# Optimization experiments

Hardware: AMD Instinct MI355X
Metric: run time of the kernel (lower is better)

The kernel has to match this reference:

```python
import jax, jax.numpy as jnp
import numpy as np

N, P, C, S, H, CLS = 32, 16, 256, 128, 4, 3000
DH = C // H
EPS = 1e-5


def setup_inputs() -> dict:
    key = jax.random.key(0)
    ks = jax.random.split(key, 8)
    sh = (N, P, C, S)
    return {
        "t_f": jax.random.normal(ks[0], sh, jnp.float32),
        "t_s": jax.random.normal(ks[1], sh, jnp.float32),
        "t_l": jax.random.normal(ks[2], sh, jnp.float32),
        # grouped 1x1 conv weights, one [out_ch, in_ch] matrix per part
        "decay_w": jax.random.normal(ks[3], (P, C, 3 * C), jnp.float32) * 0.02,
        "qkv_w": jax.random.normal(ks[4], (P, 3 * C, C), jnp.float32) * 0.02,
        "out_w": jax.random.normal(ks[5], (P, C, C), jnp.float32) * 0.02,
        # per-part BatchNorm1d affine params
        "gamma": jnp.ones((P, C), jnp.float32),
        "beta": jnp.zeros((P, C), jnp.float32),
        # classifier fc: [in_planes, class_num] (broadcast over parts)
        "fc": jax.random.normal(ks[6], (C, CLS), jnp.float32) * 0.02,
    }


def reference(t_f, t_s, t_l, decay_w, qkv_w, out_w, gamma, beta, fc):
    n, p, c, s = t_f.shape
    h, dh = H, DH
    scale = dh ** -0.5

    # decay_c: grouped 1x1 conv, 3c -> c per part
    x_cat = jnp.concatenate([t_f, t_s, t_l], axis=2)            # [n,p,3c,s]
    t_all = jnp.einsum('npis,poi->npos', x_cat, decay_w)        # [n,p,c,s]

    # Attention.to_qkv: grouped 1x1 conv, c -> 3c per part
    qkv = jnp.einsum('npcs,pqc->npqs', t_all, qkv_w)            # [n,p,3c,s]
    qkv = qkv.reshape(n, p, 3, h, dh, s).transpose(2, 0, 3, 1, 4, 5)  # [3,n,h,p,dh,s]
    q, k, v = qkv[0], qkv[1], qkv[2]

    # frame-frame attention per (head, part): [n,h,p,s,s]
    dots = jnp.einsum('nhpcs,nhpct->nhpst', q, k) * scale
    attn = jax.nn.softmax(dots, axis=-1)

    o = jnp.einsum('nhpst,nhpct->nhpcs', attn, v)               # [n,h,p,dh,s]
    o = o.transpose(0, 2, 1, 3, 4).reshape(n, p, c, s)          # [n,p,c,s]
    o = jnp.einsum('npcs,poc->npos', o, out_w)                  # to_out grouped conv

    # residual + max over frames
    wpv = (o + t_all).max(axis=-1)                              # [n,p,c]

    # select_topk_part (topk_num == 1 forced by squeeze(2) in torch code):
    # argmax over frames of column-summed attention, gather that frame of t_f, sum heads
    idx = jnp.argmax(attn.sum(axis=-2), axis=-1)                # [n,h,p]
    ib = jnp.broadcast_to(idx[:, :, :, None, None], (n, h, p, c, 1))
    sel = jnp.take_along_axis(t_f[:, None], ib, axis=-1)[..., 0]  # [n,h,p,c]
    sel = sel.sum(axis=1)                                       # [n,p,c]

    # per-part BatchNorm1d in training mode (batch statistics over n)
    mean = wpv.mean(axis=0)                                     # [p,c]
    var = wpv.var(axis=0)                                       # biased, as torch BN
    pf = (wpv - mean) / jnp.sqrt(var + EPS) * gamma + beta      # [n,p,c]

    cls = jnp.einsum('npc,ck->npk', pf, fc)                     # [n,p,class_num]
    return cls, wpv.transpose(1, 0, 2), sel.transpose(1, 0, 2)
```

## Files before the change

kernel.cpp:

```cpp
#include <hip/hip_runtime.h>
#include <math.h>

#define N_ 32
#define P_ 16
#define C_ 256
#define S_ 128
#define H_ 4
#define CLS_ 3000

typedef __attribute__((ext_vector_type(4))) float f4v;
typedef __attribute__((ext_vector_type(4))) float f32x4;
typedef __attribute__((ext_vector_type(8))) short short8;
typedef __attribute__((ext_vector_type(4))) unsigned short us4;

__device__ __forceinline__ unsigned short f2bf(float x){
    unsigned u = __float_as_uint(x);
    u += 0x7fffu + ((u >> 16) & 1u);
    return (unsigned short)(u >> 16);
}
__device__ __forceinline__ float bf2f(unsigned short h){
    return __uint_as_float(((unsigned)h) << 16);
}

typedef __attribute__((address_space(1))) const unsigned int gu32_t;
typedef __attribute__((address_space(3))) unsigned int lu32_t;
__device__ __forceinline__ void gload16(const void* g, void* l){
    __builtin_amdgcn_global_load_lds((gu32_t*)g, (lu32_t*)l, 16, 0, 0);
}

__global__ void wsplit(const float* __restrict__ dw, const float* __restrict__ qw,
                       const float* __restrict__ ow,
                       unsigned short* __restrict__ wdh, unsigned short* __restrict__ wdl,
                       unsigned short* __restrict__ wqh, unsigned short* __restrict__ wql,
                       unsigned short* __restrict__ woh){
    int i = blockIdx.x * 256 + threadIdx.x;
    int stride = gridDim.x * 256;
    for (; i < 3145728; i += stride){
        float a = dw[i]; unsigned short h = f2bf(a);
        wdh[i] = h; wdl[i] = f2bf(a - bf2f(h));
        float b = qw[i]; unsigned short h2 = f2bf(b);
        wqh[i] = h2; wql[i] = f2bf(b - bf2f(h2));
        if (i < 1048576) woh[i] = f2bf(ow[i]);
    }
}

__global__ __launch_bounds__(256) void fct_kernel(const float* __restrict__ fc,
                                                  unsigned short* __restrict__ fcT){
    int n = blockIdx.x * 256 + threadIdx.x;
    if (n < CLS_){
        for (int c = 0; c < 256; ++c) fcT[(size_t)n * 256 + c] = f2bf(fc[(size_t)c * CLS_ + n]);
    } else {
        for (int c = 0; c < 256; ++c) fcT[(size_t)n * 256 + c] = 0;
    }
}

__global__ __launch_bounds__(256) void xT_kernel(
    const float* __restrict__ t_f, const float* __restrict__ t_s,
    const float* __restrict__ t_l,
    unsigned short* __restrict__ xH, unsigned short* __restrict__ xL, int n0){
    __shared__ float T[64 * 132];
    const int np_l = blockIdx.x, tsel = blockIdx.y;
    const float* src = (tsel == 0) ? t_f : ((tsel == 1) ? t_s : t_l);
    const size_t np_g = (size_t)(n0 * 16) + np_l;
    const float* sbase = src + np_g * 256 * 128;
    const size_t dbase = (size_t)np_l * 128 * 768 + tsel * 256;
    const int tid = threadIdx.x;
    const int so = tid & 127, ch = tid >> 7;

    for (int cp = 0; cp < 4; ++cp){
        const int c0 = cp * 64;
#pragma unroll
        for (int it = 0; it < 8; ++it){
            int f = tid + 256 * it;
            int c = f >> 5, s4 = (f & 31) << 2;
            *(f4v*)(T + c * 132 + s4) = *(const f4v*)(sbase + (size_t)(c0 + c) * 128 + s4);
        }
        __syncthreads();
        short8 Hh[4], Ll[4];
#pragma unroll
        for (int c8 = 0; c8 < 4; ++c8){
#pragma unroll
            for (int j = 0; j < 8; ++j){
                float v = T[(ch * 32 + c8 * 8 + j) * 132 + so];
                unsigned short hh = f2bf(v);
                Hh[c8][j] = (short)hh;
                Ll[c8][j] = (short)f2bf(v - bf2f(hh));
            }
        }
        size_t dr = dbase + (size_t)so * 768 + c0 + ch * 32;
#pragma unroll
        for (int c8 = 0; c8 < 4; ++c8){
            *(short8*)(xH + dr + c8 * 8) = Hh[c8];
            *(short8*)(xL + dr + c8 * 8) = Ll[c8];
        }
        __syncthreads();
    }
}

template<int KEXT, int APITCH, int ND, int MODE, int OPITCH>
__global__ __launch_bounds__(256) void gemm3(
    const unsigned short* __restrict__ Ah_g, const unsigned short* __restrict__ Al_g,
    const unsigned short* __restrict__ Whi, const unsigned short* __restrict__ Wlo,
    const unsigned short* __restrict__ resH, const unsigned short* __restrict__ resL,
    unsigned short* __restrict__ outH, unsigned short* __restrict__ outL,
    float* __restrict__ outF, int n0, int cnp)
{
    constexpr int T3 = (MODE == 2) ? 0 : 1;
    constexpr int OB = ND / 128;
    __shared__ unsigned short sm[(T3 ? 4 : 2) * 128 * 64];
    unsigned short* AhL = sm;
    unsigned short* BhL = sm + 8192;
    unsigned short* AlL = T3 ? (sm + 16384) : sm;
    unsigned short* BlL = T3 ? (sm + 24576) : sm;
    unsigned short* Ep = sm;
    __shared__ float cmax[2][2][64];

    const int id = blockIdx.x;
    const int xcd = id & 7;
    const int r = id >> 3;
    const int ppl = r / (cnp * OB);
    const int rr = r % (cnp * OB);
    const int n_l = rr / OB;
    const int o_t = rr % OB;
    const int p = xcd * 2 + ppl;
    const int np_l = n_l * 16 + p;
    const int o0 = o_t * 128;

    const int tid = threadIdx.x;
    const int w = tid >> 6, l = tid & 63;
    const int lr = l & 15, lg = l >> 4;
    const int ws0 = (w & 1) * 64, wo0 = (w >> 1) * 64;
    const size_t aBase = (size_t)np_l * 128 * APITCH;
    const unsigned short* Wp_h = Whi + ((size_t)p * ND + o0) * KEXT;
    const unsigned short* Wp_l = T3 ? (Wlo + ((size_t)p * ND + o0) * KEXT) : Wp_h;

    f32x4 acc[4][4];
#pragma unroll
    for (int i = 0; i < 4; ++i)
#pragma unroll
        for (int j = 0; j < 4; ++j) acc[i][j] = (f32x4){0.f, 0.f, 0.f, 0.f};

    for (int k0 = 0; k0 < KEXT; k0 += 64){
#pragma unroll
        for (int it = 0; it < 4; ++it){
            int slot = w * 4 + it;
            int lin = slot * 64 + l;
            int row = lin >> 3, chnk = lin & 7;
            int sk = ((chnk ^ (row & 7)) << 3);
            unsigned short* ldst = sm + slot * 512;
            const unsigned short* ga = Ah_g + aBase + (size_t)row * APITCH + k0 + sk;
            gload16(ga, ldst);
            const unsigned short* gb = Wp_h + (size_t)row * KEXT + k0 + sk;
            gload16(gb, ldst + 8192);
            if (T3){
                gload16(Al_g + aBase + (size_t)row * APITCH + k0 + sk, ldst + 16384);
                gload16(Wp_l + (size_t)row * KEXT + k0 + sk, ldst + 24576);
            }
        }
        __syncthreads();
#pragma unroll
        for (int ks = 0; ks < 2; ++ks){
            short8 ah[4], al[4];
#pragma unroll
            for (int sf = 0; sf < 4; ++sf){
                int row = ws0 + sf * 16 + lr;
                int cof = ((ks * 4 + lg) ^ (row & 7)) << 3;
                ah[sf] = *(const short8*)(AhL + row * 64 + cof);
                if (T3) al[sf] = *(const short8*)(AlL + row * 64 + cof);
            }
#pragma unroll
            for (int of = 0; of < 4; ++of){
                int row = wo0 + of * 16 + lr;
                int cof = ((ks * 4 + lg) ^ (row & 7)) << 3;
                short8 bh = *(const short8*)(BhL + row * 64 + cof);
                short8 bl = bh;
                if (T3) bl = *(const short8*)(BlL + row * 64 + cof);
#pragma unroll
                for (int sf = 0; sf < 4; ++sf){
                    acc[sf][of] = __builtin_amdgcn_mfma_f32_16x16x32_bf16(ah[sf], bh, acc[sf][of], 0, 0, 0);
                    if (T3){
                        acc[sf][of] = __builtin_amdgcn_mfma_f32_16x16x32_bf16(ah[sf], bl, acc[sf][of], 0, 0, 0);
                        acc[sf][of] = __builtin_amdgcn_mfma_f32_16x16x32_bf16(al[sf], bh, acc[sf][of], 0, 0, 0);
                    }
                }
            }
        }
        __syncthreads();
    }

    if (MODE != 2){
#pragma unroll
        for (int plane = 0; plane < 2; ++plane){
#pragma unroll
            for (int sf = 0; sf < 4; ++sf)
#pragma unroll
                for (int of = 0; of < 4; ++of){
                    int col = wo0 + of * 16 + lr;
#pragma unroll
                    for (int r2 = 0; r2 < 4; ++r2){
                        int row = ws0 + sf * 16 + lg * 4 + r2;
                        float v = acc[sf][of][r2];
                        unsigned short hh = f2bf(v);
                        unsigned short q = plane ? f2bf(v - bf2f(hh)) : hh;
                        Ep[row * 136 + col] = q;
                    }
                }
            __syncthreads();
            unsigned short* dst = plane ? outL : outH;
#pragma unroll
            for (int it = 0; it < 8; ++it){
                int idx = tid + 256 * it;
                int row = idx >> 4, seg = (idx & 15) * 8;
                *(short8*)(dst + (size_t)np_l * 128 * OPITCH + (size_t)row * OPITCH + o0 + seg) =
                    *(const short8*)(Ep + row * 136 + seg);
            }
            __syncthreads();
        }
    } else {
        const int n_g = n0 + n_l;
#pragma unroll
        for (int of = 0; of < 4; ++of){
            int oc = o0 + wo0 + of * 16 + lr;
            float m = -INFINITY;
#pragma unroll
            for (int sf = 0; sf < 4; ++sf){
#pragma unroll
                for (int r2 = 0; r2 < 4; ++r2){
                    int s = ws0 + sf * 16 + lg * 4 + r2;
                    size_t ri = (size_t)np_l * 128 * 256 + (size_t)s * 256 + oc;
                    float v = acc[sf][of][r2] + bf2f(resH[ri]) + bf2f(resL[ri]);
                    m = fmaxf(m, v);
                }
            }
            m = fmaxf(m, __shfl_xor(m, 16));
            m = fmaxf(m, __shfl_xor(m, 32));
            if (l < 16) cmax[w >> 1][w & 1][of * 16 + l] = m;
        }
        __syncthreads();
        if (tid < 128){
            int oh = tid >> 6, col = tid & 63;
            float v = fmaxf(cmax[oh][0][col], cmax[oh][1][col]);
            outF[((size_t)p * N_ + n_g) * C_ + o0 + oh * 64 + col] = v;
        }
    }
}

__global__ __launch_bounds__(256) void attn3(unsigned short* __restrict__ qH,
                                             const unsigned short* __restrict__ qL,
                                             int* __restrict__ idxA, int n0, int cnp){
    __shared__ char smraw[17408 + 34816 + 2048];
    unsigned short* Vs = (unsigned short*)smraw;
    unsigned short* Pm = (unsigned short*)(smraw + 17408);
    float* csW = (float*)(smraw + 17408 + 34816);
    unsigned short* Ot = (unsigned short*)smraw;

    const int id = blockIdx.x;
    const int xcd = id & 7;
    const int r = id >> 3;
    const int ppl = r / (cnp * 4);
    const int rr = r % (cnp * 4);
    const int n_l = rr >> 2, h = rr & 3;
    const int p = xcd * 2 + ppl;
    const int np_l = n_l * 16 + p;
    const int tid = threadIdx.x, w = tid >> 6, l = tid & 63;
    const int lr = l & 15, lg = l >> 4;
    unsigned short* baseH = qH + (size_t)np_l * 128 * 768;
    const unsigned short* baseL = qL + (size_t)np_l * 128 * 768;

#pragma unroll
    for (int it = 0; it < 8; ++it){
        int idx = tid + 256 * it;
        int t = idx >> 4, d4 = (idx & 15) * 4;
        us4 v = *(const us4*)(baseH + (size_t)t * 768 + 512 + h * 64 + d4);
#pragma unroll
        for (int j = 0; j < 4; ++j) Vs[(d4 + j) * 136 + t] = v[j];
    }

    short8 qh[2][2], ql[2][2];
#pragma unroll
    for (int sf = 0; sf < 2; ++sf)
#pragma unroll
        for (int ks = 0; ks < 2; ++ks){
            size_t off = (size_t)(w * 32 + sf * 16 + lr) * 768 + h * 64 + ks * 32 + lg * 8;
            qh[sf][ks] = *(const short8*)(baseH + off);
            ql[sf][ks] = *(const short8*)(baseL + off);
        }

    f32x4 dacc[2][8];
#pragma unroll
    for (int i = 0; i < 2; ++i)
#pragma unroll
        for (int j = 0; j < 8; ++j) dacc[i][j] = (f32x4){0.f, 0.f, 0.f, 0.f};

#pragma unroll
    for (int tf = 0; tf < 8; ++tf){
#pragma unroll
        for (int ks = 0; ks < 2; ++ks){
            size_t off = (size_t)(tf * 16 + lr) * 768 + 256 + h * 64 + ks * 32 + lg * 8;
            short8 kh = *(const short8*)(baseH + off);
            short8 kl = *(const short8*)(baseL + off);
#pragma unroll
            for (int sf = 0; sf < 2; ++sf){
                dacc[sf][tf] = __builtin_amdgcn_mfma_f32_16x16x32_bf16(qh[sf][ks], kh, dacc[sf][tf], 0, 0, 0);
                dacc[sf][tf] = __builtin_amdgcn_mfma_f32_16x16x32_bf16(qh[sf][ks], kl, dacc[sf][tf], 0, 0, 0);
                dacc[sf][tf] = __builtin_amdgcn_mfma_f32_16x16x32_bf16(ql[sf][ks], kh, dacc[sf][tf], 0, 0, 0);
            }
        }
    }

    float csp[8];
#pragma unroll
    for (int tf = 0; tf < 8; ++tf) csp[tf] = 0.f;
#pragma unroll
    for (int sf = 0; sf < 2; ++sf){
#pragma unroll
        for (int r2 = 0; r2 < 4; ++r2){
            float m = -INFINITY;
#pragma unroll
            for (int tf = 0; tf < 8; ++tf) m = fmaxf(m, dacc[sf][tf][r2]);
            m = fmaxf(m, __shfl_xor(m, 1)); m = fmaxf(m, __shfl_xor(m, 2));
            m = fmaxf(m, __shfl_xor(m, 4)); m = fmaxf(m, __shfl_xor(m, 8));
            float e[8]; float sum = 0.f;
#pragma unroll
            for (int tf = 0; tf < 8; ++tf){
                e[tf] = __expf(0.125f * (dacc[sf][tf][r2] - m)); sum += e[tf];
            }
            sum += __shfl_xor(sum, 1); sum += __shfl_xor(sum, 2);
            sum += __shfl_xor(sum, 4); sum += __shfl_xor(sum, 8);
            float inv = 1.f / sum;
            int s = w * 32 + sf * 16 + lg * 4 + r2;
#pragma unroll
            for (int tf = 0; tf < 8; ++tf){
                float pv = e[tf] * inv;
                Pm[s * 136 + tf * 16 + lr] = f2bf(pv);
                csp[tf] += pv;
            }
        }
    }
#pragma unroll
    for (int tf = 0; tf < 8; ++tf){
        float v = csp[tf];
        v += __shfl_xor(v, 16); v += __shfl_xor(v, 32);
        if (l < 16) csW[w * 128 + tf * 16 + l] = v;
    }
    __syncthreads();

    f32x4 oacc[8];
#pragma unroll
    for (int i = 0; i < 8; ++i) oacc[i] = (f32x4){0.f, 0.f, 0.f, 0.f};
#pragma unroll
    for (int ks = 0; ks < 4; ++ks){
        short8 av = *(const short8*)(Vs + (w * 16 + lr) * 136 + ks * 32 + lg * 8);
#pragma unroll
        for (int sf = 0; sf < 8; ++sf){
            short8 bp = *(const short8*)(Pm + (sf * 16 + lr) * 136 + ks * 32 + lg * 8);
            oacc[sf] = __builtin_amdgcn_mfma_f32_16x16x32_bf16(av, bp, oacc[sf], 0, 0, 0);
        }
    }
    __syncthreads();

    if (tid < 64){
        float v0 = csW[tid] + csW[128 + tid] + csW[256 + tid] + csW[384 + tid];
        float v1 = csW[64 + tid] + csW[192 + tid] + csW[320 + tid] + csW[448 + tid];
        float bv; int bi;
        if (v1 > v0){ bv = v1; bi = 64 + tid; } else { bv = v0; bi = tid; }
#pragma unroll
        for (int msk = 1; msk <= 32; msk <<= 1){
            float ov = __shfl_xor(bv, msk); int oi = __shfl_xor(bi, msk);
            if (ov > bv || (ov == bv && oi < bi)){ bv = ov; bi = oi; }
        }
        if (tid == 0){ int n_g = n0 + n_l; idxA[(n_g * H_ + h) * P_ + p] = bi; }
    }

#pragma unroll
    for (int sf = 0; sf < 8; ++sf){
        int s = sf * 16 + lr;
#pragma unroll
        for (int r2 = 0; r2 < 4; ++r2) Ot[s * 72 + w * 16 + lg * 4 + r2] = f2bf(oacc[sf][r2]);
    }
    __syncthreads();
#pragma unroll
    for (int it = 0; it < 4; ++it){
        int idx = tid + 256 * it;
        int s = idx >> 3, d8 = (idx & 7) * 8;
        *(short8*)(baseH + (size_t)s * 768 + h * 64 + d8) = *(const short8*)(Ot + s * 72 + d8);
    }
}

__global__ void bn_stats(const float* __restrict__ wpvT,
                         const float* __restrict__ gamma,
                         const float* __restrict__ beta,
                         float* __restrict__ aArr, float* __restrict__ bArr)
{
    int i = blockIdx.x * blockDim.x + threadIdx.x;
    if (i >= P_ * C_) return;
    int p = i / C_, c = i % C_;
    const float* basep = wpvT + (size_t)p * N_ * C_ + c;
    float su = 0.f, s2 = 0.f;
    for (int n = 0; n < N_; ++n){
        float v = basep[n * C_];
        su += v; s2 += v * v;
    }
    float mean = su * (1.f / N_);
    float var = s2 * (1.f / N_) - mean * mean;
    float rstd = rsqrtf(var + 1e-5f);
    float a = gamma[i] * rstd;
    aArr[i] = a;
    bArr[i] = beta[i] - mean * a;
}

__global__ __launch_bounds__(256) void pf_kernel(const float* __restrict__ wpvT,
                                                 const float* __restrict__ aArr,
                                                 const float* __restrict__ bArr,
                                                 unsigned short* __restrict__ pfb){
    int m = blockIdx.x, c = threadIdx.x;
    int p = m >> 5;
    float v = wpvT[(size_t)m * 256 + c];
    pfb[(size_t)m * 256 + c] = f2bf(v * aArr[p * 256 + c] + bArr[p * 256 + c]);
}

__global__ __launch_bounds__(256) void gemmc(const unsigned short* __restrict__ pfb,
                                             const unsigned short* __restrict__ fcT,
                                             float* __restrict__ cls){
    __shared__ unsigned short sm[2 * 128 * 72];
    unsigned short* AhL = sm;
    unsigned short* BhL = sm + 128 * 72;

    const int tid = threadIdx.x;
    const int w = tid >> 6, l = tid & 63;
    const int lr = l & 15, lg = l >> 4;
    const int ws0 = (w & 1) * 64, wo0 = (w >> 1) * 64;
    const int o0 = blockIdx.x * 128;
    const int m0 = blockIdx.y * 128;

    f32x4 acc[4][4];
#pragma unroll
    for (int i = 0; i < 4; ++i)
#pragma unroll
        for (int j = 0; j < 4; ++j) acc[i][j] = (f32x4){0.f, 0.f, 0.f, 0.f};

    for (int k0 = 0; k0 < 256; k0 += 64){
#pragma unroll
        for (int it = 0; it < 4; ++it){
            int idx = tid + 256 * it;
            int s = idx >> 3, c8 = (idx & 7) * 8;
            *(short8*)(AhL + s * 72 + c8) = *(const short8*)(pfb + (size_t)(m0 + s) * 256 + k0 + c8);
            *(short8*)(BhL + s * 72 + c8) = *(const short8*)(fcT + (size_t)(o0 + s) * 256 + k0 + c8);
        }
        __syncthreads();
#pragma unroll
        for (int ks = 0; ks < 2; ++ks){
            short8 ah[4];
#pragma unroll
            for (int sf = 0; sf < 4; ++sf)
                ah[sf] = *(const short8*)(AhL + (ws0 + sf * 16 + lr) * 72 + ks * 32 + lg * 8);
#pragma unroll
            for (int of = 0; of < 4; ++of){
                short8 bh = *(const short8*)(BhL + (wo0 + of * 16 + lr) * 72 + ks * 32 + lg * 8);
#pragma unroll
                for (int sf = 0; sf < 4; ++sf)
                    acc[sf][of] = __builtin_amdgcn_mfma_f32_16x16x32_bf16(ah[sf], bh, acc[sf][of], 0, 0, 0);
            }
        }
        __syncthreads();
    }
#pragma unroll
    for (int sf = 0; sf < 4; ++sf)
#pragma unroll
        for (int of = 0; of < 4; ++of){
            int oc = o0 + wo0 + of * 16 + lr;
            if (oc < CLS_){
#pragma unroll
                for (int r2 = 0; r2 < 4; ++r2){
                    int m = m0 + ws0 + sf * 16 + lg * 4 + r2;
                    int n = m & 31, p = m >> 5;
                    cls[((size_t)n * 16 + p) * CLS_ + oc] = acc[sf][of][r2];
                }
            }
        }
}

__global__ void sel_kernel(const float* __restrict__ t_f,
                           const int* __restrict__ idxArr,
                           float* __restrict__ selT)
{
    const int np = blockIdx.x;
    const int n = np >> 4, p = np & 15;
    const int c = threadIdx.x;
    float acc = 0.f;
#pragma unroll
    for (int h = 0; h < H_; ++h){
        int s = idxArr[(n * H_ + h) * P_ + p];
        acc += t_f[((size_t)np * C_ + c) * S_ + s];
    }
    selT[((size_t)p * N_ + n) * C_ + c] = acc;
}

extern "C" void kernel_launch(void* const* d_in, const int* in_sizes, int n_in,
                              void* d_out, int out_size, void* d_ws, size_t ws_size,
                              hipStream_t stream)
{
    const float* t_f     = (const float*)d_in[0];
    const float* t_s     = (const float*)d_in[1];
    const float* t_l     = (const float*)d_in[2];
    const float* decay_w = (const float*)d_in[3];
    const float* qkv_w   = (const float*)d_in[4];
    const float* out_w   = (const float*)d_in[5];
    const float* gamma   = (const float*)d_in[6];
    const float* beta    = (const float*)d_in[7];
    const float* fc      = (const float*)d_in[8];
    float* out = (float*)d_out;

    const size_t WD = 3145728, WQ = 3145728, WO = 1048576;
    char* basep = (char*)d_ws;
    unsigned short* wdh = (unsigned short*)basep;
    unsigned short* wdl = wdh + WD;
    unsigned short* wqh = wdl + WD;
    unsigned short* wql = wqh + WQ;
    unsigned short* woh = wql + WQ;
    unsigned short* fcT = woh + WO;
    unsigned short* pfb = fcT + 3072 * 256;
    float* aArr = (float*)(pfb + 512 * 256);
    float* bArr = aArr + P_ * C_;
    int* idxA = (int*)(bArr + P_ * C_);
    char* big = (char*)(idxA + N_ * H_ * P_);
    size_t head = (size_t)(big - basep);
    size_t avail = (ws_size > head) ? (ws_size - head) : 0;
    const size_t per_n = (size_t)16 * 128 * (768 + 256 + 768) * 2 * 2;
    int cn = (int)(avail / per_n);
    if (cn < 1) cn = 1;
    if (cn > N_) cn = N_;
    int nch = (N_ + cn - 1) / cn;
    cn = (N_ + nch - 1) / nch;

    unsigned short* xH = (unsigned short*)big;
    unsigned short* xL = xH + (size_t)cn * 16 * 128 * 768;
    unsigned short* tH = xL + (size_t)cn * 16 * 128 * 768;
    unsigned short* tL = tH + (size_t)cn * 16 * 128 * 256;
    unsigned short* qH = tL + (size_t)cn * 16 * 128 * 256;
    unsigned short* qL = qH + (size_t)cn * 16 * 128 * 768;

    float* cls  = out;
    float* wpvT = out + (size_t)N_ * P_ * CLS_;
    float* selT = wpvT + (size_t)P_ * N_ * C_;

    wsplit<<<2048, 256, 0, stream>>>(decay_w, qkv_w, out_w, wdh, wdl, wqh, wql, woh);
    fct_kernel<<<12, 256, 0, stream>>>(fc, fcT);

    for (int n0 = 0; n0 < N_; n0 += cn){
        int c = (N_ - n0 < cn) ? (N_ - n0) : cn;
        int npg = c * 16;
        xT_kernel<<<dim3(npg, 3), 256, 0, stream>>>(t_f, t_s, t_l, xH, xL, n0);
        gemm3<768, 768, 256, 0, 256><<<npg * 2, 256, 0, stream>>>(
            xH, xL, wdh, wdl, nullptr, nullptr, tH, tL, nullptr, n0, c);
        gemm3<256, 256, 768, 1, 768><<<npg * 6, 256, 0, stream>>>(
            tH, tL, wqh, wql, nullptr, nullptr, qH, qL, nullptr, n0, c);
        attn3<<<c * 64, 256, 0, stream>>>(qH, qL, idxA, n0, c);
        gemm3<256, 768, 256, 2, 256><<<npg * 2, 256, 0, stream>>>(
            qH, qH, woh, woh, tH, tL, nullptr, nullptr, wpvT, n0, c);
    }
    bn_stats<<<(P_ * C_ + 255) / 256, 256, 0, stream>>>(wpvT, gamma, beta, aArr, bArr);
    pf_kernel<<<512, 256, 0, stream>>>(wpvT, aArr, bArr, pfb);
    gemmc<<<dim3(24, 4), 256, 0, stream>>>(pfb, fcT, cls);
    sel_kernel<<<N_ * P_, 256, 0, stream>>>(t_f, idxA, selT);
}
```

Baseline: 522.8 us.

## Fuse input transpose and bf16 split into the decay GEMM

Removes the separate xT_kernel, which transposed the fp32 inputs and wrote hi/lo bf16 copies to workspace. The new gemm0t kernel loads fp32 tiles of t_f/t_s/t_l directly, converts and transposes them in shared memory, and runs the 3-term split-bf16 MFMA product against the decay weights. This cuts a full write and reread of the expanded input buffers and frees workspace so larger n-chunks fit. The cost is an extra barrier and in-LDS conversion per k-step, no double buffering, and the fp32 global loads sit on the GEMM's critical path.

```diff
diff --git a/kernel.cpp b/kernel.cpp
--- a/kernel.cpp
+++ b/kernel.cpp
@@ -54,44 +54,136 @@
     }
 }
 
-__global__ __launch_bounds__(256) void xT_kernel(
+__global__ __launch_bounds__(256) void gemm0t(
     const float* __restrict__ t_f, const float* __restrict__ t_s,
     const float* __restrict__ t_l,
-    unsigned short* __restrict__ xH, unsigned short* __restrict__ xL, int n0){
-    __shared__ float T[64 * 132];
-    const int np_l = blockIdx.x, tsel = blockIdx.y;
-    const float* src = (tsel == 0) ? t_f : ((tsel == 1) ? t_s : t_l);
-    const size_t np_g = (size_t)(n0 * 16) + np_l;
-    const float* sbase = src + np_g * 256 * 128;
-    const size_t dbase = (size_t)np_l * 128 * 768 + tsel * 256;
+    const unsigned short* __restrict__ Whi, const unsigned short* __restrict__ Wlo,
+    unsigned short* __restrict__ outH, unsigned short* __restrict__ outL,
+    int n0, int cnp)
+{
+    __shared__ unsigned short sm[24576];
+    float* Tf = (float*)sm;
+    unsigned short* AhL = sm + 8192;
+    unsigned short* AlL = sm + 12288;
+    unsigned short* BhL = sm + 16384;
+    unsigned short* BlL = sm + 20480;
+    unsigned short* Ep  = sm;
+
+    const int id = blockIdx.x;
+    const int xcd = id & 7;
+    const int r = id >> 3;
+    const int ppl = r / (cnp * 2);
+    const int rr = r % (cnp * 2);
+    const int n_l = rr >> 1;
+    const int o_t = rr & 1;
+    const int p = xcd * 2 + ppl;
+    const int np_l = n_l * 16 + p;
+    const int o0 = o_t * 128;
+    const size_t np_g = (size_t)(n0 + n_l) * 16 + p;
+
     const int tid = threadIdx.x;
-    const int so = tid & 127, ch = tid >> 7;
-
-    for (int cp = 0; cp < 4; ++cp){
-        const int c0 = cp * 64;
+    const int w = tid >> 6, l = tid & 63;
+    const int lr = l & 15, lg = l >> 4;
+    const int ws0 = (w & 1) * 64, wo0 = (w >> 1) * 64;
+    const int s2 = tid & 127, khalf = tid >> 7;
+
+    const unsigned short* Wp_h = Whi + ((size_t)p * 256 + o0) * 768;
+    const unsigned short* Wp_l = Wlo + ((size_t)p * 256 + o0) * 768;
+
+    f32x4 acc[4][4];
+#pragma unroll
+    for (int i = 0; i < 4; ++i)
+#pragma unroll
+        for (int j = 0; j < 4; ++j) acc[i][j] = (f32x4){0.f, 0.f, 0.f, 0.f};
+
+    for (int k0 = 0; k0 < 768; k0 += 32){
+        const int t = k0 >> 8;
+        const float* src = (t == 0) ? t_f : ((t == 1) ? t_s : t_l);
+        const float* xbase = src + (np_g * 256 + (k0 & 255)) * 128;
+#pragma unroll
+        for (int it = 0; it < 4; ++it){
+            int lin = (w * 4 + it) * 64 + l;
+            gload16(xbase + lin * 4, Tf + lin * 4);
+        }
+#pragma unroll
+        for (int it = 0; it < 2; ++it){
+            int lin = (w * 2 + it) * 64 + l;
+            int row = lin >> 2, ch = lin & 3;
+            int sk = ((ch ^ ((row >> 1) & 3)) << 3);
+            gload16(Wp_h + (size_t)row * 768 + k0 + sk, BhL + lin * 8);
+            gload16(Wp_l + (size_t)row * 768 + k0 + sk, BlL + lin * 8);
+        }
+        __syncthreads();
+        {
+            short8 h0, h1, l0, l1;
+#pragma unroll
+            for (int j = 0; j < 8; ++j){
+                float v = Tf[(khalf * 16 + j) * 128 + s2];
+                unsigned short hh = f2bf(v);
+                h0[j] = (short)hh; l0[j] = (short)f2bf(v - bf2f(hh));
+            }
+#pragma unroll
+            for (int j = 0; j < 8; ++j){
+                float v = Tf[(khalf * 16 + 8 + j) * 128 + s2];
+                unsigned short hh = f2bf(v);
+                h1[j] = (short)hh; l1[j] = (short)f2bf(v - bf2f(hh));
+            }
+            int sb = (s2 >> 1) & 3;
+            int c0 = (khalf * 2) ^ sb, c1 = (khalf * 2 + 1) ^ sb;
+            *(short8*)(AhL + s2 * 32 + c0 * 8) = h0;
+            *(short8*)(AhL + s2 * 32 + c1 * 8) = h1;
+            *(short8*)(AlL + s2 * 32 + c0 * 8) = l0;
+            *(short8*)(AlL + s2 * 32 + c1 * 8) = l1;
+        }
+        __syncthreads();
+        short8 ah[4], al[4];
+#pragma unroll
+        for (int sf = 0; sf < 4; ++sf){
+            int row = ws0 + sf * 16 + lr;
+            int cof = (lg ^ ((row >> 1) & 3)) << 3;
+            ah[sf] = *(const short8*)(AhL + row * 32 + cof);
+            al[sf] = *(const short8*)(AlL + row * 32 + cof);
+        }
+#pragma unroll
+        for (int of = 0; of < 4; ++of){
+            int row = wo0 + of * 16 + lr;
+            int cof = (lg ^ ((row >> 1) & 3)) << 3;
+            short8 bh = *(const short8*)(BhL + row * 32 + cof);
+            short8 bl = *(const short8*)(BlL + row * 32 + cof);
+#pragma unroll
+            for (int sf = 0; sf < 4; ++sf){
+                acc[sf][of] = __builtin_amdgcn_mfma_f32_16x16x32_bf16(ah[sf], bh, acc[sf][of], 0, 0, 0);
+                acc[sf][of] = __builtin_amdgcn_mfma_f32_16x16x32_bf16(ah[sf], bl, acc[sf][of], 0, 0, 0);
+                acc[sf][of] = __builtin_amdgcn_mfma_f32_16x16x32_bf16(al[sf], bh, acc[sf][of], 0, 0, 0);
+            }
+        }
+        __syncthreads();
+    }
+
+#pragma unroll
+    for (int plane = 0; plane < 2; ++plane){
+#pragma unroll
+        for (int sf = 0; sf < 4; ++sf)
+#pragma unroll
+            for (int of = 0; of < 4; ++of){
+                int col = wo0 + of * 16 + lr;
+#pragma unroll
+                for (int r2 = 0; r2 < 4; ++r2){
+                    int row = ws0 + sf * 16 + lg * 4 + r2;
+                    float v = acc[sf][of][r2];
+                    unsigned short hh = f2bf(v);
+                    unsigned short q = plane ? f2bf(v - bf2f(hh)) : hh;
+                    Ep[row * 136 + col] = q;
+                }
+            }
+        __syncthreads();
+        unsigned short* dst = plane ? outL : outH;
 #pragma unroll
         for (int it = 0; it < 8; ++it){
-            int f = tid + 256 * it;
-            int c = f >> 5, s4 = (f & 31) << 2;
-            *(f4v*)(T + c * 132 + s4) = *(const f4v*)(sbase + (size_t)(c0 + c) * 128 + s4);
-        }
-        __syncthreads();
-        short8 Hh[4], Ll[4];
-#pragma unroll
-        for (int c8 = 0; c8 < 4; ++c8){
-#pragma unroll
-            for (int j = 0; j < 8; ++j){
-                float v = T[(ch * 32 + c8 * 8 + j) * 132 + so];
-                unsigned short hh = f2bf(v);
-                Hh[c8][j] = (short)hh;
-                Ll[c8][j] = (short)f2bf(v - bf2f(hh));
-            }
-        }
-        size_t dr = dbase + (size_t)so * 768 + c0 + ch * 32;
-#pragma unroll
-        for (int c8 = 0; c8 < 4; ++c8){
-            *(short8*)(xH + dr + c8 * 8) = Hh[c8];
-            *(short8*)(xL + dr + c8 * 8) = Ll[c8];
+            int idx = tid + 256 * it;
+            int row = idx >> 4, seg = (idx & 15) * 8;
+            *(short8*)(dst + (size_t)np_l * 128 * 256 + (size_t)row * 256 + o0 + seg) =
+                *(const short8*)(Ep + row * 136 + seg);
         }
         __syncthreads();
     }
@@ -526,16 +618,14 @@
     char* big = (char*)(idxA + N_ * H_ * P_);
     size_t head = (size_t)(big - basep);
     size_t avail = (ws_size > head) ? (ws_size - head) : 0;
-    const size_t per_n = (size_t)16 * 128 * (768 + 256 + 768) * 2 * 2;
+    const size_t per_n = (size_t)16 * 128 * (256 + 768) * 2 * 2;
     int cn = (int)(avail / per_n);
     if (cn < 1) cn = 1;
     if (cn > N_) cn = N_;
     int nch = (N_ + cn - 1) / cn;
     cn = (N_ + nch - 1) / nch;
 
-    unsigned short* xH = (unsigned short*)big;
-    unsigned short* xL = xH + (size_t)cn * 16 * 128 * 768;
-    unsigned short* tH = xL + (size_t)cn * 16 * 128 * 768;
+    unsigned short* tH = (unsigned short*)big;
     unsigned short* tL = tH + (size_t)cn * 16 * 128 * 256;
     unsigned short* qH = tL + (size_t)cn * 16 * 128 * 256;
     unsigned short* qL = qH + (size_t)cn * 16 * 128 * 768;
@@ -550,9 +640,8 @@
     for (int n0 = 0; n0 < N_; n0 += cn){
         int c = (N_ - n0 < cn) ? (N_ - n0) : cn;
         int npg = c * 16;
-        xT_kernel<<<dim3(npg, 3), 256, 0, stream>>>(t_f, t_s, t_l, xH, xL, n0);
-        gemm3<768, 768, 256, 0, 256><<<npg * 2, 256, 0, stream>>>(
-            xH, xL, wdh, wdl, nullptr, nullptr, tH, tL, nullptr, n0, c);
+        gemm0t<<<npg * 2, 256, 0, stream>>>(
+            t_f, t_s, t_l, wdh, wdl, tH, tL, n0, c);
         gemm3<256, 256, 768, 1, 768><<<npg * 6, 256, 0, stream>>>(
             tH, tL, wqh, wql, nullptr, nullptr, qH, qL, nullptr, n0, c);
         attn3<<<c * 64, 256, 0, stream>>>(qH, qL, idxA, n0, c);
```

After: 439.5 us. 1.19x faster.
